# Optimization experiments

Measured on AMD Instinct MI355X. Metric: run time of the kernel, lower is better.

The kernel has to match this reference:

```python
import jax, jax.numpy as jnp
import numpy as np

HIDDEN = 768
MLP_HIDDEN = 3072
HEADS = 12
HEAD_DIM = HIDDEN // HEADS

def setup_inputs() -> dict:
    key = jax.random.key(0)
    ks = jax.random.split(key, 12)
    s = 0.02
    return {
        "x": jax.random.normal(ks[0], (16, 1024, HIDDEN), dtype=jnp.float32),
        "ln1_g": jnp.ones((HIDDEN,), jnp.float32),
        "ln1_b": jnp.zeros((HIDDEN,), jnp.float32),
        "wq": jax.random.normal(ks[1], (HIDDEN, HIDDEN), jnp.float32) * s,
        "wk": jax.random.normal(ks[2], (HIDDEN, HIDDEN), jnp.float32) * s,
        "wv": jax.random.normal(ks[3], (HIDDEN, HIDDEN), jnp.float32) * s,
        "wo": jax.random.normal(ks[4], (HIDDEN, HIDDEN), jnp.float32) * s,
        "bo": jnp.zeros((HIDDEN,), jnp.float32),
        "ln2_g": jnp.ones((HIDDEN,), jnp.float32),
        "ln2_b": jnp.zeros((HIDDEN,), jnp.float32),
        "w1": jax.random.normal(ks[5], (HIDDEN, MLP_HIDDEN), jnp.float32) * s,
        "b1": jnp.zeros((MLP_HIDDEN,), jnp.float32),
        "w2": jax.random.normal(ks[6], (MLP_HIDDEN, HIDDEN), jnp.float32) * s,
        "b2": jnp.zeros((HIDDEN,), jnp.float32),
    }

def _layernorm(x, g, b, eps=1e-5):
    mu = jnp.mean(x, axis=-1, keepdims=True)
    var = jnp.mean(jnp.square(x - mu), axis=-1, keepdims=True)
    return (x - mu) * jax.lax.rsqrt(var + eps) * g + b

def reference(x, ln1_g, ln1_b, wq, wk, wv, wo, bo, ln2_g, ln2_b, w1, b1, w2, b2):
    b, n, _ = x.shape
    h, d = HEADS, HEAD_DIM
    scale = d ** -0.5
    # Attention branch
    xn = _layernorm(x, ln1_g, ln1_b)
    q = (xn @ wq.T).reshape(b, n, h, d).transpose(0, 2, 1, 3)  # bhnd
    k = (xn @ wk.T).reshape(b, n, h, d).transpose(0, 2, 1, 3)
    v = (xn @ wv.T).reshape(b, n, h, d).transpose(0, 2, 1, 3)
    score = jax.nn.softmax(jnp.einsum('bhif,bhjf->bhij', q, k) * scale, axis=-1)
    attn = jnp.einsum('bhij,bhjf->bihf', score, v).reshape(b, n, h * d)
    x = attn @ wo.T + bo + x
    # MLP branch
    xn = _layernorm(x, ln2_g, ln2_b)
    hdn = jax.nn.gelu(xn @ w1 + b1, approximate=False)
    x = hdn @ w2 + b2 + x
    return x
```

## Files before the change

### kernel.cpp

```cpp
#include <hip/hip_runtime.h>
#include <hip/hip_bf16.h>

#define HIDDEN 768
#define MLPH   3072
#define HEADS  12
#define HD     64
#define SEQ    1024
#define BATCH  16
#define MTOT   (BATCH*SEQ)

typedef __attribute__((ext_vector_type(8))) short  short8;
typedef __attribute__((ext_vector_type(4))) short  short4x;
typedef __attribute__((ext_vector_type(8))) __bf16 bf16x8;
typedef __attribute__((ext_vector_type(4))) float  floatx4;

#define CL2 0.18033688011112042f

__device__ inline short f2bf(float f) {
  __hip_bfloat16 h = __float2bfloat16(f);
  return *reinterpret_cast<short*>(&h);
}

__device__ inline floatx4 mfma_bf16(short8 a, short8 b, floatx4 c) {
  return __builtin_amdgcn_mfma_f32_16x16x32_bf16(
      __builtin_bit_cast(bf16x8, a), __builtin_bit_cast(bf16x8, b), c, 0, 0, 0);
}

__device__ inline void gl_lds16(const short* g, short* l) {
  __builtin_amdgcn_global_load_lds(
      (const __attribute__((address_space(1))) unsigned int*)g,
      (__attribute__((address_space(3))) unsigned int*)l, 16, 0, 0);
}

__device__ inline float gelu_f(float x) {
  float z = 0.7978845608028654f * (x + 0.044715f * x * x * x);
  float e = __builtin_amdgcn_exp2f(z * 2.8853900817779268f);
  float t = 1.0f - 2.0f * __builtin_amdgcn_rcpf(e + 1.0f);
  return 0.5f * x * (1.0f + t);
}

__global__ __launch_bounds__(256) void conv_weights(
    const float* __restrict__ wq, const float* __restrict__ wk,
    const float* __restrict__ wv, const float* __restrict__ wo,
    short* __restrict__ wqkvb, short* __restrict__ wob)
{
  int i = blockIdx.x * 256 + threadIdx.x;
  const int HH = HIDDEN * HIDDEN;
  if (i < HH) {
    wqkvb[i]        = f2bf(wq[i] * CL2);
    wqkvb[HH + i]   = f2bf(wk[i]);
    wqkvb[2*HH + i] = f2bf(wv[i]);
    wob[i]          = f2bf(wo[i]);
  }
}

__global__ __launch_bounds__(256) void wtrans_kernel(
    const float* __restrict__ in, short* __restrict__ out, int RK, int CN)
{
  __shared__ float T[64][65];
  int n0 = blockIdx.x * 64, k0 = blockIdx.y * 64;
  int tx = threadIdx.x & 63, ty = threadIdx.x >> 6;
#pragma unroll
  for (int r = ty; r < 64; r += 4)
    T[r][tx] = in[(size_t)(k0 + r) * CN + n0 + tx];
  __syncthreads();
#pragma unroll
  for (int r = ty; r < 64; r += 4)
    out[(size_t)(n0 + r) * RK + k0 + tx] = f2bf(T[tx][r]);
}

__global__ __launch_bounds__(192) void ln_kernel(
    const float* __restrict__ x, const float* __restrict__ g,
    const float* __restrict__ b, short* __restrict__ out)
{
  int row = blockIdx.x;
  int t = threadIdx.x;
  float4 v = ((const float4*)(x + (size_t)row * HIDDEN))[t];
  float s  = (v.x + v.y) + (v.z + v.w);
  float s2 = (v.x*v.x + v.y*v.y) + (v.z*v.z + v.w*v.w);
  for (int off = 32; off > 0; off >>= 1) {
    s  += __shfl_down(s, off);
    s2 += __shfl_down(s2, off);
  }
  __shared__ float red[6];
  __shared__ float stats[2];
  int wave = t >> 6;
  if ((t & 63) == 0) { red[wave] = s; red[3 + wave] = s2; }
  __syncthreads();
  if (t == 0) {
    float S  = red[0] + red[1] + red[2];
    float S2 = red[3] + red[4] + red[5];
    float mu  = S * (1.0f / HIDDEN);
    float var = S2 * (1.0f / HIDDEN) - mu * mu;
    stats[0] = mu;
    stats[1] = rsqrtf(var + 1e-5f);
  }
  __syncthreads();
  float mu = stats[0], rs = stats[1];
  float4 gv = ((const float4*)g)[t];
  float4 bv = ((const float4*)b)[t];
  short4x o;
  o[0] = f2bf((v.x - mu) * rs * gv.x + bv.x);
  o[1] = f2bf((v.y - mu) * rs * gv.y + bv.y);
  o[2] = f2bf((v.z - mu) * rs * gv.z + bv.z);
  o[3] = f2bf((v.w - mu) * rs * gv.w + bv.w);
  *(short4x*)(out + (size_t)row * HIDDEN + t * 4) = o;
}

template<int OUTMODE , bool BIAS, bool GELU_E, bool RES,
         bool VSPLIT = false>
__global__ __launch_bounds__(512, 2) void gemm_bt2(
    const short* __restrict__ A, const short* __restrict__ B,
    const float* __restrict__ bias, const float* __restrict__ res,
    void* __restrict__ out, short* __restrict__ vout, int M, int N, int K)
{
  __shared__ alignas(16) short As[2][2][8192];
  __shared__ alignas(16) short Bs[2][2][8192];

  int tid = threadIdx.x;
  int lane = tid & 63, wave = tid >> 6;
  int wr = wave >> 2, wc = wave & 3;
  int quad = lane >> 4, lc = lane & 15;

  int nbx = gridDim.x;
  int nwg = nbx * gridDim.y;
  int orig = blockIdx.y * nbx + blockIdx.x;
  int q8 = nwg >> 3, r8 = nwg & 7;
  int xcd = orig & 7, sub = orig >> 3;
  int wg = (xcd < r8 ? xcd * (q8 + 1) : r8 * (q8 + 1) + (xcd - r8) * q8) + sub;
  int m0 = (wg / nbx) * 256;
  int n0 = (wg % nbx) * 256;

  int srow = tid >> 2;
  int skb  = (tid & 3) ^ ((srow >> 1) & 3);
  const short* ga = A + (size_t)(m0 + srow) * K + skb * 8;
  const short* gb = B + (size_t)(n0 + srow) * K + skb * 8;
  const size_t rowskip = (size_t)128 * K;
  int lb0 = wave * 512;

#define STAGE_R(MAT, gp, sl, ks, kt) {                         \
    const short* _g = (gp) + (size_t)(kt) * 64 + (ks) * 32;    \
    gl_lds16(_g,           &MAT[sl][ks][lb0]);                 \
    gl_lds16(_g + rowskip, &MAT[sl][ks][4096 + lb0]);          \
  }

  floatx4 acc[8][4];
#pragma unroll
  for (int i = 0; i < 8; ++i)
#pragma unroll
    for (int j = 0; j < 4; ++j) acc[i][j] = floatx4{0.f, 0.f, 0.f, 0.f};

  int apos = (quad ^ ((lc >> 1) & 3)) * 8;
#define RD(buf, r) (*(const short8*)&(buf)[(r) * 32 + apos])
#define MM4x4(IOFF)                                                     \
    _Pragma("unroll")                                                   \
    for (int i = 0; i < 4; ++i)                                         \
      _Pragma("unroll")                                                 \
      for (int j = 0; j < 4; ++j)                                       \
        acc[i + IOFF][j] = mfma_bf16(aF[i], bF[j], acc[i + IOFF][j]);

  int NK = K >> 6;

  STAGE_R(As, ga, 0, 0, 0); STAGE_R(Bs, gb, 0, 0, 0);
  STAGE_R(As, ga, 0, 1, 0); STAGE_R(Bs, gb, 0, 1, 0);

  for (int kt = 0; kt < NK; ++kt) {
    const int sl = kt & 1;
    const short (*as_)[8192] = As[sl];
    const short (*bs_)[8192] = Bs[sl];
    const int s2 = sl ^ 1;
    const bool st = (kt + 1 < NK);
    short8 aF[4], bF[4];

    asm volatile("s_waitcnt vmcnt(2)" ::: "memory");
    __builtin_amdgcn_s_barrier();
    asm volatile("" ::: "memory");
#pragma unroll
    for (int i = 0; i < 4; ++i) aF[i] = RD(as_[0], wr * 128 + i * 16 + lc);
#pragma unroll
    for (int j = 0; j < 4; ++j) bF[j] = RD(bs_[0], wc * 64 + j * 16 + lc);
    if (st) STAGE_R(Bs, gb, s2, 1, kt + 1);
    asm volatile("s_waitcnt lgkmcnt(0)" ::: "memory");
    __builtin_amdgcn_sched_barrier(0);
    __builtin_amdgcn_s_setprio(1);
    MM4x4(0);
    __builtin_amdgcn_s_setprio(0);

    __builtin_amdgcn_s_barrier();
    asm volatile("" ::: "memory");
#pragma unroll
    for (int i = 0; i < 4; ++i) aF[i] = RD(as_[0], wr * 128 + (i + 4) * 16 + lc);
    if (st) STAGE_R(Bs, gb, s2, 0, kt + 1);
    asm volatile("s_waitcnt lgkmcnt(0)" ::: "memory");
    __builtin_amdgcn_sched_barrier(0);
    __builtin_amdgcn_s_setprio(1);
    MM4x4(4);
    __builtin_amdgcn_s_setprio(0);

    if (st) asm volatile("s_waitcnt vmcnt(4)" ::: "memory");
    else    asm volatile("s_waitcnt vmcnt(0)" ::: "memory");
    __builtin_amdgcn_s_barrier();
    asm volatile("" ::: "memory");
#pragma unroll
    for (int i = 0; i < 4; ++i) aF[i] = RD(as_[1], wr * 128 + i * 16 + lc);
#pragma unroll
    for (int j = 0; j < 4; ++j) bF[j] = RD(bs_[1], wc * 64 + j * 16 + lc);
    if (st) STAGE_R(As, ga, s2, 0, kt + 1);
    asm volatile("s_waitcnt lgkmcnt(0)" ::: "memory");
    __builtin_amdgcn_sched_barrier(0);
    __builtin_amdgcn_s_setprio(1);
    MM4x4(0);
    __builtin_amdgcn_s_setprio(0);

    __builtin_amdgcn_s_barrier();
    asm volatile("" ::: "memory");
#pragma unroll
    for (int i = 0; i < 4; ++i) aF[i] = RD(as_[1], wr * 128 + (i + 4) * 16 + lc);
    if (st) STAGE_R(As, ga, s2, 1, kt + 1);
    asm volatile("s_waitcnt lgkmcnt(0)" ::: "memory");
    __builtin_amdgcn_sched_barrier(0);
    __builtin_amdgcn_s_setprio(1);
    MM4x4(4);
    __builtin_amdgcn_s_setprio(0);
  }
#undef STAGE_R
#undef RD
#undef MM4x4

#pragma unroll
  for (int i = 0; i < 8; ++i)
#pragma unroll
    for (int j = 0; j < 4; ++j)
#pragma unroll
      for (int r = 0; r < 4; ++r) {
        int row = m0 + wr * 128 + i * 16 + quad * 4 + r;
        int col = n0 + wc * 64 + j * 16 + lc;
        float v = acc[i][j][r];
        if (BIAS)   v += bias[col];
        if (GELU_E) v = gelu_f(v);
        if (RES)    v += res[(size_t)row * N + col];
        if (VSPLIT && col >= 2 * HIDDEN) {
          int b_ = row >> 10, rr = row & 1023, kt_ = rr >> 6, k_ = rr & 63;
          int ks_ = k_ >> 5, kk = k_ & 31;
          int hd = col - 2 * HIDDEN, h_ = hd >> 6, d_ = hd & 63;
          size_t idx = ((size_t)((b_ * HEADS + h_) * 16 + kt_)) * 4096
                     + ks_ * 2048 + d_ * 32
                     + (((kk >> 3) ^ ((d_ >> 1) & 3)) << 3) + (kk & 7);
          vout[idx] = f2bf(v);
        } else if (OUTMODE == 1) {
          ((short*)out)[(size_t)row * N + col] = f2bf(v);
        } else {
          ((float*)out)[(size_t)row * N + col] = v;
        }
      }
}

__global__ __launch_bounds__(512) void attn_kernel(
    const short* __restrict__ qkv, const short* __restrict__ vtg,
    short* __restrict__ out)
{
  int NB = gridDim.x * gridDim.y * gridDim.z;
  int L  = (blockIdx.z * gridDim.y + blockIdx.y) * gridDim.x + blockIdx.x;
  int xcd = L & 7, s = L >> 3;
  int per = NB >> 6;
  int bh  = xcd * per + (s >> 3);
  int qt  = s & 7;
  int h   = bh % HEADS;
  int b   = bh / HEADS;
  int tid = threadIdx.x, lane = tid & 63, wave = tid >> 6;
  int quad = lane >> 4, lc = lane & 15;

  __shared__ alignas(16) short Qs[2 * 128 * 32];
  __shared__ alignas(16) short Ks[2][4096];
  __shared__ alignas(16) short Vs[2][4096];
  __shared__ alignas(16) short Ps[8][16 * 72];

  const int LDQ = 3 * HIDDEN;
  const short* qb = qkv + (size_t)(b * SEQ) * LDQ + h * HD;
  const short* kb = qb + HIDDEN;
  const short* vt = vtg + (size_t)((b * HEADS + h) * 16) * 4096;

  {
    int row = tid >> 2, blk = tid & 3;
    int kblk = blk ^ ((row >> 1) & 3);
#pragma unroll
    for (int t = 0; t < 2; ++t) {
      const short* g = qb + (size_t)(qt * 128 + row) * LDQ + t * 32 + kblk * 8;
      gl_lds16(g, &Qs[t * 4096 + wave * 512]);
    }
  }
  int srow = (tid >> 2) & 63;
  int sks  = tid >> 8;
  int skb  = (tid & 3) ^ ((srow >> 1) & 3);
  const short* kg0 = kb + (size_t)srow * LDQ + sks * 32 + skb * 8;
  const short* vg0 = vt + tid * 8;
  gl_lds16(kg0, &Ks[0][wave * 512]);
  gl_lds16(vg0, &Vs[0][wave * 512]);
  __syncthreads();

  int pos = quad ^ ((lc >> 1) & 3);
  short8 aq[2];
#pragma unroll
  for (int ks = 0; ks < 2; ++ks)
    aq[ks] = *(const short8*)&Qs[ks * 4096 + (wave * 16 + lc) * 32 + pos * 8];

  floatx4 oacc[4];
#pragma unroll
  for (int n2 = 0; n2 < 4; ++n2) oacc[n2] = floatx4{0.f, 0.f, 0.f, 0.f};
  float lsum = 0.f;
  short* pw = &Ps[wave][0];

  for (int kt = 0; kt < 16; ++kt) {
    const int sl = kt & 1;
    if (kt) {
      asm volatile("s_waitcnt vmcnt(0)" ::: "memory");
      __builtin_amdgcn_s_barrier();
      asm volatile("" ::: "memory");
    }
    if (kt + 1 < 16) {
      gl_lds16(kg0 + (size_t)((kt + 1) * 64) * LDQ, &Ks[sl ^ 1][wave * 512]);
      gl_lds16(vg0 + (kt + 1) * 4096, &Vs[sl ^ 1][wave * 512]);
    }

    floatx4 sacc[4];
#pragma unroll
    for (int m2 = 0; m2 < 4; ++m2) sacc[m2] = floatx4{0.f, 0.f, 0.f, 0.f};
#pragma unroll
    for (int ks = 0; ks < 2; ++ks) {
#pragma unroll
      for (int m2 = 0; m2 < 4; ++m2) {
        short8 ak = *(const short8*)&Ks[sl][ks * 2048 + (m2 * 16 + lc) * 32 + pos * 8];
        sacc[m2] = mfma_bf16(ak, aq[ks], sacc[m2]);
      }
    }

#pragma unroll
    for (int m2 = 0; m2 < 4; ++m2) {
      float p0 = exp2f(sacc[m2][0]);
      float p1 = exp2f(sacc[m2][1]);
      float p2 = exp2f(sacc[m2][2]);
      float p3 = exp2f(sacc[m2][3]);
      lsum += (p0 + p1) + (p2 + p3);
      short4x pk;
      pk[0] = f2bf(p0); pk[1] = f2bf(p1); pk[2] = f2bf(p2); pk[3] = f2bf(p3);
      *(short4x*)&pw[lc * 72 + m2 * 16 + quad * 4] = pk;
    }
    asm volatile("s_waitcnt lgkmcnt(0)" ::: "memory");
    __builtin_amdgcn_sched_barrier(0);

#pragma unroll
    for (int ks = 0; ks < 2; ++ks) {
      short8 ap = *(const short8*)&pw[lc * 72 + (ks * 4 + quad) * 8];
#pragma unroll
      for (int n2 = 0; n2 < 4; ++n2) {
        short8 bv = *(const short8*)&Vs[sl][ks * 2048 + (n2 * 16 + lc) * 32 + pos * 8];
        oacc[n2] = mfma_bf16(ap, bv, oacc[n2]);
      }
    }
  }

  float rs = lsum;
  rs += __shfl_xor(rs, 16);
  rs += __shfl_xor(rs, 32);
#pragma unroll
  for (int r = 0; r < 4; ++r) {
    float inv = 1.0f / __shfl(rs, quad * 4 + r);
    int row = b * SEQ + qt * 128 + wave * 16 + quad * 4 + r;
#pragma unroll
    for (int n2 = 0; n2 < 4; ++n2) {
      int col = h * HD + n2 * 16 + lc;
      out[(size_t)row * HIDDEN + col] = f2bf(oacc[n2][r] * inv);
    }
  }
}

extern "C" void kernel_launch(void* const* d_in, const int* in_sizes, int n_in,
                              void* d_out, int out_size, void* d_ws, size_t ws_size,
                              hipStream_t stream) {
  const float* x    = (const float*)d_in[0];
  const float* ln1g = (const float*)d_in[1];
  const float* ln1b = (const float*)d_in[2];
  const float* wq   = (const float*)d_in[3];
  const float* wk   = (const float*)d_in[4];
  const float* wv   = (const float*)d_in[5];
  const float* wo   = (const float*)d_in[6];
  const float* bo   = (const float*)d_in[7];
  const float* ln2g = (const float*)d_in[8];
  const float* ln2b = (const float*)d_in[9];
  const float* w1   = (const float*)d_in[10];
  const float* b1   = (const float*)d_in[11];
  const float* w2   = (const float*)d_in[12];
  const float* b2   = (const float*)d_in[13];

  auto rup = [](size_t b) { return (b + 255) & ~(size_t)255; };

  int R = SEQ;
  const int cands[4] = {16384, 8192, 4096, 2048};
  {
    const size_t wbytes = rup((size_t)3 * HIDDEN * HIDDEN * 2) +
                          rup((size_t)HIDDEN * HIDDEN * 2) +
                          rup((size_t)MLPH * HIDDEN * 2) +
                          rup((size_t)HIDDEN * MLPH * 2);
    for (int i = 0; i < 4; ++i) {
      size_t need = wbytes + rup((size_t)cands[i] * 1536) + rup((size_t)cands[i] * 6144)
                           + rup((size_t)cands[i] * 1536);
      if (need <= ws_size) { R = cands[i]; break; }
    }
  }

  char* ws = (char*)d_ws;
  size_t off = 0;
  auto alloc = [&](size_t bytes) {
    char* p = ws + off;
    off += (bytes + 255) & ~(size_t)255;
    return p;
  };
  short* wqkvb = (short*)alloc((size_t)3 * HIDDEN * HIDDEN * 2);
  short* wob   = (short*)alloc((size_t)HIDDEN * HIDDEN * 2);
  short* w1t   = (short*)alloc((size_t)MLPH * HIDDEN * 2);
  short* w2t   = (short*)alloc((size_t)HIDDEN * MLPH * 2);
  short* slotA = (short*)alloc((size_t)R * 1536);
  short* bigR  = (short*)alloc((size_t)R * 6144);
  short* vtg   = (short*)alloc((size_t)R * 1536);

  conv_weights<<<(HIDDEN * HIDDEN + 255) / 256, 256, 0, stream>>>(
      wq, wk, wv, wo, wqkvb, wob);
  wtrans_kernel<<<dim3(MLPH / 64, HIDDEN / 64), 256, 0, stream>>>(
      w1, w1t, HIDDEN, MLPH);
  wtrans_kernel<<<dim3(HIDDEN / 64, MLPH / 64), 256, 0, stream>>>(
      w2, w2t, MLPH, HIDDEN);

  const int nch = MTOT / R;
  for (int c = 0; c < nch; ++c) {
    const float* xc  = x + (size_t)c * R * HIDDEN;
    float*       x2c = (float*)d_out + (size_t)c * R * HIDDEN;

    ln_kernel<<<R, 192, 0, stream>>>(xc, ln1g, ln1b, slotA);
    gemm_bt2<1, false, false, false, true>
        <<<dim3((3 * HIDDEN) / 256, R / 256), 512, 0, stream>>>(
        slotA, wqkvb, nullptr, nullptr, bigR, vtg, R, 3 * HIDDEN, HIDDEN);
    attn_kernel<<<dim3(SEQ / 128, HEADS, R / SEQ), 512, 0, stream>>>(
        bigR, vtg, slotA);
    gemm_bt2<0, true, false, true>
        <<<dim3(HIDDEN / 256, R / 256), 512, 0, stream>>>(
        slotA, wob, bo, xc, x2c, nullptr, R, HIDDEN, HIDDEN);
    ln_kernel<<<R, 192, 0, stream>>>(x2c, ln2g, ln2b, slotA);
    gemm_bt2<1, true, true, false>
        <<<dim3(MLPH / 256, R / 256), 512, 0, stream>>>(
        slotA, w1t, b1, nullptr, bigR, nullptr, R, MLPH, HIDDEN);
    gemm_bt2<0, true, false, true>
        <<<dim3(HIDDEN / 256, R / 256), 512, 0, stream>>>(
        bigR, w2t, b2, x2c, x2c, nullptr, R, HIDDEN, MLPH);
  }
}
```

Before: 554.5 us.

## Switch GEMM to triple-buffered K=32 slices with two-ahead prefetch

The GEMM main loop moves from double-buffered K=64 tiles (two K=32 halves per stage) to a three-slot ring of K=32 slices, prefetching two slices ahead. The aim is to hide global-to-LDS load latency better, since each slot has more compute time before it is reused. LDS use drops from 64KB to 48KB per block. The price is twice as many loop iterations, with more barriers and waitcnts per unit of K work, plus modulo-3 slot arithmetic.

```diff
diff --git a/kernel.cpp b/kernel.cpp
--- a/kernel.cpp
+++ b/kernel.cpp
@@ -114,8 +114,8 @@
     const float* __restrict__ bias, const float* __restrict__ res,
     void* __restrict__ out, short* __restrict__ vout, int M, int N, int K)
 {
-  __shared__ alignas(16) short As[2][2][8192];
-  __shared__ alignas(16) short Bs[2][2][8192];
+  __shared__ alignas(16) short As[3][8192];
+  __shared__ alignas(16) short Bs[3][8192];
 
   int tid = threadIdx.x;
   int lane = tid & 63, wave = tid >> 6;
@@ -138,10 +138,15 @@
   const size_t rowskip = (size_t)128 * K;
   int lb0 = wave * 512;
 
-#define STAGE_R(MAT, gp, sl, ks, kt) {                         \
-    const short* _g = (gp) + (size_t)(kt) * 64 + (ks) * 32;    \
-    gl_lds16(_g,           &MAT[sl][ks][lb0]);                 \
-    gl_lds16(_g + rowskip, &MAT[sl][ks][4096 + lb0]);          \
+#define STAGE_A(SL, KT) {                                      \
+    const short* _g = ga + (size_t)(KT) * 32;                  \
+    gl_lds16(_g,           &As[SL][lb0]);                      \
+    gl_lds16(_g + rowskip, &As[SL][4096 + lb0]);               \
+  }
+#define STAGE_B(SL, KT) {                                      \
+    const short* _g = gb + (size_t)(KT) * 32;                  \
+    gl_lds16(_g,           &Bs[SL][lb0]);                      \
+    gl_lds16(_g + rowskip, &Bs[SL][4096 + lb0]);               \
   }
 
   floatx4 acc[8][4];
@@ -159,27 +164,28 @@
       for (int j = 0; j < 4; ++j)                                       \
         acc[i + IOFF][j] = mfma_bf16(aF[i], bF[j], acc[i + IOFF][j]);
 
-  int NK = K >> 6;
-
-  STAGE_R(As, ga, 0, 0, 0); STAGE_R(Bs, gb, 0, 0, 0);
-  STAGE_R(As, ga, 0, 1, 0); STAGE_R(Bs, gb, 0, 1, 0);
-
+  int NK = K >> 5;
+
+  STAGE_A(0, 0); STAGE_B(0, 0);
+  STAGE_A(1, 1); STAGE_B(1, 1);
+
+  int sl = 0;
   for (int kt = 0; kt < NK; ++kt) {
-    const int sl = kt & 1;
-    const short (*as_)[8192] = As[sl];
-    const short (*bs_)[8192] = Bs[sl];
-    const int s2 = sl ^ 1;
-    const bool st = (kt + 1 < NK);
+    int s2 = sl + 2; if (s2 >= 3) s2 -= 3;
+    const short* as_ = As[sl];
+    const short* bs_ = Bs[sl];
+    const bool st = (kt + 2 < NK);
     short8 aF[4], bF[4];
 
-    asm volatile("s_waitcnt vmcnt(2)" ::: "memory");
+    if (kt + 1 < NK) asm volatile("s_waitcnt vmcnt(4)" ::: "memory");
+    else             asm volatile("s_waitcnt vmcnt(0)" ::: "memory");
     __builtin_amdgcn_s_barrier();
     asm volatile("" ::: "memory");
 #pragma unroll
-    for (int i = 0; i < 4; ++i) aF[i] = RD(as_[0], wr * 128 + i * 16 + lc);
-#pragma unroll
-    for (int j = 0; j < 4; ++j) bF[j] = RD(bs_[0], wc * 64 + j * 16 + lc);
-    if (st) STAGE_R(Bs, gb, s2, 1, kt + 1);
+    for (int i = 0; i < 4; ++i) aF[i] = RD(as_, wr * 128 + i * 16 + lc);
+#pragma unroll
+    for (int j = 0; j < 4; ++j) bF[j] = RD(bs_, wc * 64 + j * 16 + lc);
+    if (st) STAGE_A(s2, kt + 2);
     asm volatile("s_waitcnt lgkmcnt(0)" ::: "memory");
     __builtin_amdgcn_sched_barrier(0);
     __builtin_amdgcn_s_setprio(1);
@@ -189,41 +195,18 @@
     __builtin_amdgcn_s_barrier();
     asm volatile("" ::: "memory");
 #pragma unroll
-    for (int i = 0; i < 4; ++i) aF[i] = RD(as_[0], wr * 128 + (i + 4) * 16 + lc);
-    if (st) STAGE_R(Bs, gb, s2, 0, kt + 1);
+    for (int i = 0; i < 4; ++i) aF[i] = RD(as_, wr * 128 + (i + 4) * 16 + lc);
+    if (st) STAGE_B(s2, kt + 2);
     asm volatile("s_waitcnt lgkmcnt(0)" ::: "memory");
     __builtin_amdgcn_sched_barrier(0);
     __builtin_amdgcn_s_setprio(1);
     MM4x4(4);
     __builtin_amdgcn_s_setprio(0);
 
-    if (st) asm volatile("s_waitcnt vmcnt(4)" ::: "memory");
-    else    asm volatile("s_waitcnt vmcnt(0)" ::: "memory");
-    __builtin_amdgcn_s_barrier();
-    asm volatile("" ::: "memory");
-#pragma unroll
-    for (int i = 0; i < 4; ++i) aF[i] = RD(as_[1], wr * 128 + i * 16 + lc);
-#pragma unroll
-    for (int j = 0; j < 4; ++j) bF[j] = RD(bs_[1], wc * 64 + j * 16 + lc);
-    if (st) STAGE_R(As, ga, s2, 0, kt + 1);
-    asm volatile("s_waitcnt lgkmcnt(0)" ::: "memory");
-    __builtin_amdgcn_sched_barrier(0);
-    __builtin_amdgcn_s_setprio(1);
-    MM4x4(0);
-    __builtin_amdgcn_s_setprio(0);
-
-    __builtin_amdgcn_s_barrier();
-    asm volatile("" ::: "memory");
-#pragma unroll
-    for (int i = 0; i < 4; ++i) aF[i] = RD(as_[1], wr * 128 + (i + 4) * 16 + lc);
-    if (st) STAGE_R(As, ga, s2, 1, kt + 1);
-    asm volatile("s_waitcnt lgkmcnt(0)" ::: "memory");
-    __builtin_amdgcn_sched_barrier(0);
-    __builtin_amdgcn_s_setprio(1);
-    MM4x4(4);
-    __builtin_amdgcn_s_setprio(0);
-  }
-#undef STAGE_R
+    sl = sl + 1; if (sl == 3) sl = 0;
+  }
+#undef STAGE_A
+#undef STAGE_B
 #undef RD
 #undef MM4x4
 
```

Result: no change. 561.5 us (+1.3%).
